# Kernel tuning notes

Measured on AMD Instinct MI355X. Metric: run time of the kernel, lower is better.

## Reference

```python
import jax, jax.numpy as jnp
import numpy as np

RADIUS = 8
EPS = 0.01


def _xdiff(h, r):
    # box-sum along H (axis 2) from cumsum via shifted-slice differences
    l = h[:, :, r:2 * r + 1]
    m = h[:, :, 2 * r + 1:] - h[:, :, :-2 * r - 1]
    rr = h[:, :, -1:] - h[:, :, -2 * r - 1:-r - 1]
    return jnp.concatenate([l, m, rr], axis=2)


def _ydiff(h, r):
    # box-sum along W (axis 3)
    l = h[:, :, :, r:2 * r + 1]
    m = h[:, :, :, 2 * r + 1:] - h[:, :, :, :-2 * r - 1]
    rr = h[:, :, :, -1:] - h[:, :, :, -2 * r - 1:-r - 1]
    return jnp.concatenate([l, m, rr], axis=3)


def mean_filter(x, r):
    return _ydiff(jnp.cumsum(_xdiff(jnp.cumsum(x, axis=2), r), axis=3), r)


def setup_inputs() -> dict:
    key = jax.random.key(0)
    k1, k2 = jax.random.split(key)
    shape = (8, 3, 1024, 1024)
    x = jax.random.uniform(k1, shape, dtype=jnp.float32)
    y = jax.random.uniform(k2, shape, dtype=jnp.float32)
    return {"x": x, "y": y}


def reference(x, y):
    r = RADIUS
    b, c, h, w = x.shape
    mask = jnp.ones((1, 1, h, w), dtype=x.dtype)
    nump = mean_filter(mask, r)  # per-pixel window counts (handles borders)
    x_mean = mean_filter(x, r) / nump
    y_mean = mean_filter(y, r) / nump
    xy_cov = mean_filter(x * y, r) / nump - x_mean * y_mean
    x_var = mean_filter(x * x, r) / nump - x_mean * x_mean
    a = xy_cov / (x_var + EPS)
    a_mean = mean_filter(a, r) / nump
    b_mean = mean_filter(y_mean - a * x_mean, r) / nump
    return a_mean * x + b_mean
```

## Files before the change

kernel.cpp:

```cpp
#include <hip/hip_runtime.h>


namespace {
constexpr int RAD  = 8;
constexpr int H    = 1024;
constexpr int W    = 1024;
constexpr int NSL  = 24;
constexpr int ROWS = 32;
constexpr int PW   = W + 2 * RAD;
constexpr float EPS_C = 0.01f;
constexpr int GRID = NSL * (H / ROWS);
constexpr size_t IMG = (size_t)NSL * H * W;
}

__device__ __forceinline__ float frcp(float v) { return __builtin_amdgcn_rcpf(v); }
__device__ __forceinline__ float4 z4() { return make_float4(0.f, 0.f, 0.f, 0.f); }

struct V4 { float4 x, y, xy, xx; };

__device__ __forceinline__ void vzero(V4& S) { S.x = z4(); S.y = z4(); S.xy = z4(); S.xx = z4(); }

__device__ __forceinline__ void vadd(V4& S, const float4 xv, const float4 yv) {
  S.x.x += xv.x; S.x.y += xv.y; S.x.z += xv.z; S.x.w += xv.w;
  S.y.x += yv.x; S.y.y += yv.y; S.y.z += yv.z; S.y.w += yv.w;
  S.xy.x += xv.x * yv.x; S.xy.y += xv.y * yv.y; S.xy.z += xv.z * yv.z; S.xy.w += xv.w * yv.w;
  S.xx.x += xv.x * xv.x; S.xx.y += xv.y * xv.y; S.xx.z += xv.z * xv.z; S.xx.w += xv.w * xv.w;
}

__device__ __forceinline__ void vsub(V4& S, const float4 xv, const float4 yv) {
  S.x.x -= xv.x; S.x.y -= xv.y; S.x.z -= xv.z; S.x.w -= xv.w;
  S.y.x -= yv.x; S.y.y -= yv.y; S.y.z -= yv.z; S.y.w -= yv.w;
  S.xy.x -= xv.x * yv.x; S.xy.y -= xv.y * yv.y; S.xy.z -= xv.z * yv.z; S.xy.w -= xv.w * yv.w;
  S.xx.x -= xv.x * xv.x; S.xx.y -= xv.y * xv.y; S.xx.z -= xv.z * xv.z; S.xx.w -= xv.w * xv.w;
}

__device__ __forceinline__ void map_block(int g, int& slice, int& r0) {
  const int xcd = g & 7;
  const int i = g >> 3;
  const int band = xcd * 4 + (i & 3);
  slice = i >> 2;
  r0 = band * ROWS;
}

__device__ __forceinline__ void hbox(const float* buf, int c0, float o[4]) {
  const float4 va = *reinterpret_cast<const float4*>(buf + c0);
  const float4 vb = *reinterpret_cast<const float4*>(buf + c0 + 4);
  const float4 vc = *reinterpret_cast<const float4*>(buf + c0 + 8);
  const float4 vd = *reinterpret_cast<const float4*>(buf + c0 + 12);
  const float4 ve = *reinterpret_cast<const float4*>(buf + c0 + 16);
  const float w[20] = {va.x, va.y, va.z, va.w, vb.x, vb.y, vb.z, vb.w,
                       vc.x, vc.y, vc.z, vc.w, vd.x, vd.y, vd.z, vd.w,
                       ve.x, ve.y, ve.z, ve.w};
  float s = w[0];
#pragma unroll
  for (int k = 1; k <= 16; ++k) s += w[k];
  o[0] = s;
  o[1] = o[0] - w[0] + w[17];
  o[2] = o[1] - w[1] + w[18];
  o[3] = o[2] - w[2] + w[19];
}

__device__ __forceinline__ float inv_cnt(int p) {
  int lo = p - RAD < 0 ? 0 : p - RAD;
  int hi = p + RAD > H - 1 ? H - 1 : p + RAD;
  return frcp((float)(hi - lo + 1));
}

__device__ __forceinline__ float4 ldrow(const float* __restrict__ s, int r, int c0) {
  return *reinterpret_cast<const float4*>(s + (size_t)r * W + c0);
}

__device__ __forceinline__ void publish(float* fbase, int c0, const V4& S) {
  *reinterpret_cast<float4*>(&fbase[0 * PW + RAD + c0]) = S.x;
  *reinterpret_cast<float4*>(&fbase[1 * PW + RAD + c0]) = S.y;
  *reinterpret_cast<float4*>(&fbase[2 * PW + RAD + c0]) = S.xy;
  *reinterpret_cast<float4*>(&fbase[3 * PW + RAD + c0]) = S.xx;
}

__device__ __forceinline__ void compute_ab(const float* fbase, int c0, float invcy,
                                           const float invcx[4], float av[4], float bv[4]) {
  float bx[4], by[4], bxy[4], bxx[4];
  hbox(fbase + 0 * PW, c0, bx);
  hbox(fbase + 1 * PW, c0, by);
  hbox(fbase + 2 * PW, c0, bxy);
  hbox(fbase + 3 * PW, c0, bxx);
#pragma unroll
  for (int j = 0; j < 4; ++j) {
    const float invN = invcy * invcx[j];
    const float mx = bx[j] * invN;
    const float my = by[j] * invN;
    const float cov = bxy[j] * invN - mx * my;
    const float var = bxx[j] * invN - mx * mx;
    const float a = cov * frcp(var + EPS_C);
    av[j] = a;
    bv[j] = my - a * mx;
  }
}

__device__ __forceinline__ void publish2(float* sbase, int c0, const float av[4], const float bv[4]) {
  *reinterpret_cast<float4*>(&sbase[RAD + c0]) = make_float4(av[0], av[1], av[2], av[3]);
  *reinterpret_cast<float4*>(&sbase[PW + RAD + c0]) = make_float4(bv[0], bv[1], bv[2], bv[3]);
}

__device__ __forceinline__ void hbox2(const float* sbase, int c0, float HA[4], float HB[4]) {
  hbox(sbase, c0, HA);
  hbox(sbase + PW, c0, HB);
}

__device__ __forceinline__ void setup_invcx(int c0, float invcx[4]) {
#pragma unroll
  for (int j = 0; j < 4; ++j) {
    const int c = c0 + j;
    const int cl = c - RAD < 0 ? 0 : c - RAD;
    const int ch = c + RAD > W - 1 ? W - 1 : c + RAD;
    invcx[j] = frcp((float)(ch - cl + 1));
  }
}

__global__ __launch_bounds__(256, 3) void k_ab(
    const float* __restrict__ x, const float* __restrict__ y,
    float* __restrict__ ag, float* __restrict__ bg) {
  __shared__ float stage[4 * PW];

  const int t = threadIdx.x;
  int slice, r0;
  map_block(blockIdx.x, slice, r0);
  const size_t soff = (size_t)slice * H * W;
  const float* xs = x + soff;
  const float* ys = y + soff;
  float* as = ag + soff;
  float* bs = bg + soff;
  const int c0 = t << 2;

  if (t < 64) {
    const int j = t >> 4, q = t & 15;
    const int pos = (q < 8) ? q : (W + RAD + (q - 8));
    stage[j * PW + pos] = 0.f;
  }

  float invcx[4];
  setup_invcx(c0, invcx);

  V4 SL; vzero(SL);
  {
    int lo = r0 - RAD < 0 ? 0 : r0 - RAD;
    for (int rr = lo; rr <= r0 + RAD; ++rr)
      vadd(SL, ldrow(xs, rr, c0), ldrow(ys, rr, c0));
  }
  __syncthreads();

  for (int p = r0; p < r0 + ROWS; ++p) {
    float4 xa = z4(), ya = z4(), xr = z4(), yr = z4();
    if (p + 9 <= H - 1) { xa = ldrow(xs, p + 9, c0); ya = ldrow(ys, p + 9, c0); }
    if (p - RAD >= 0)   { xr = ldrow(xs, p - RAD, c0); yr = ldrow(ys, p - RAD, c0); }

    publish(stage, c0, SL);
    __syncthreads();

    float av[4], bv[4];
    compute_ab(stage, c0, inv_cnt(p), invcx, av, bv);
    *reinterpret_cast<float4*>(as + (size_t)p * W + c0) = make_float4(av[0], av[1], av[2], av[3]);
    *reinterpret_cast<float4*>(bs + (size_t)p * W + c0) = make_float4(bv[0], bv[1], bv[2], bv[3]);

    vadd(SL, xa, ya);
    vsub(SL, xr, yr);
    __syncthreads();
  }
}

__global__ __launch_bounds__(256, 3) void k_out(
    const float* __restrict__ ag, const float* __restrict__ bg,
    const float* __restrict__ x, float* __restrict__ out) {
  __shared__ float srow[2 * PW];

  const int t = threadIdx.x;
  int slice, r0;
  map_block(blockIdx.x, slice, r0);
  const size_t soff = (size_t)slice * H * W;
  const float* as = ag + soff;
  const float* bs = bg + soff;
  const float* xs = x + soff;
  float* os = out + soff;
  const int c0 = t << 2;

  if (t < 32) {
    const int j = t >> 4, q = t & 15;
    const int pos = (q < 8) ? q : (W + RAD + (q - 8));
    srow[j * PW + pos] = 0.f;
  }

  float invcx[4];
  setup_invcx(c0, invcx);

  float4 Va = z4(), Vb = z4();
  {
    int lo = r0 - RAD < 0 ? 0 : r0 - RAD;
    for (int rr = lo; rr <= r0 + RAD; ++rr) {
      const float4 a4 = ldrow(as, rr, c0);
      const float4 b4 = ldrow(bs, rr, c0);
      Va.x += a4.x; Va.y += a4.y; Va.z += a4.z; Va.w += a4.w;
      Vb.x += b4.x; Vb.y += b4.y; Vb.z += b4.z; Vb.w += b4.w;
    }
  }
  __syncthreads();

  for (int k = r0; k < r0 + ROWS; ++k) {
    const float4 xk = ldrow(xs, k, c0);
    float4 aa = z4(), ba = z4(), ar = z4(), br = z4();
    if (k + 9 <= H - 1) { aa = ldrow(as, k + 9, c0); ba = ldrow(bs, k + 9, c0); }
    if (k - RAD >= 0)   { ar = ldrow(as, k - RAD, c0); br = ldrow(bs, k - RAD, c0); }

    *reinterpret_cast<float4*>(&srow[0 * PW + RAD + c0]) = Va;
    *reinterpret_cast<float4*>(&srow[1 * PW + RAD + c0]) = Vb;
    __syncthreads();

    float HA[4], HB[4];
    hbox(srow, c0, HA);
    hbox(srow + PW, c0, HB);

    const float invcy = inv_cnt(k);
    const float n0 = invcy * invcx[0], n1 = invcy * invcx[1];
    const float n2 = invcy * invcx[2], n3 = invcy * invcx[3];
    float4 o;
    o.x = HA[0] * n0 * xk.x + HB[0] * n0;
    o.y = HA[1] * n1 * xk.y + HB[1] * n1;
    o.z = HA[2] * n2 * xk.z + HB[2] * n2;
    o.w = HA[3] * n3 * xk.w + HB[3] * n3;
    *reinterpret_cast<float4*>(os + (size_t)k * W + c0) = o;

    Va.x += aa.x - ar.x; Va.y += aa.y - ar.y; Va.z += aa.z - ar.z; Va.w += aa.w - ar.w;
    Vb.x += ba.x - br.x; Vb.y += ba.y - br.y; Vb.z += ba.z - br.z; Vb.w += ba.w - br.w;
    __syncthreads();
  }
}

__global__ __launch_bounds__(256, 3) void k_fused(
    const float* __restrict__ x, const float* __restrict__ y, float* __restrict__ out) {
  __shared__ float stage[12 * PW];
  float* fL = stage;
  float* fG = stage + 4 * PW;
  float* sL = stage + 8 * PW;
  float* sG = stage + 10 * PW;

  const int t = threadIdx.x;
  int slice, r0;
  map_block(blockIdx.x, slice, r0);
  const size_t soff = (size_t)slice * H * W;
  const float* xs = x + soff;
  const float* ys = y + soff;
  float* os = out + soff;
  const int c0 = t << 2;

  if (t < 96) {
    const int j = t >> 3, tt = t & 7;
    stage[j * PW + tt] = 0.f;
    stage[j * PW + W + RAD + tt] = 0.f;
  }

  float invcx[4];
  setup_invcx(c0, invcx);

  const int cstart = (r0 - 9 < 0) ? 0 : (r0 - 9);
  V4 SL; vzero(SL);
  {
    int lo = cstart - RAD; if (lo < 0) lo = 0;
    for (int rr = lo; rr <= cstart + RAD; ++rr) {
      vadd(SL, ldrow(xs, rr, c0), ldrow(ys, rr, c0));
    }
  }
  V4 SG;
  if (r0 == 0) vzero(SG); else SG = SL;
  float4 Sa = z4(), Sb = z4();

  __syncthreads();

  for (int c = cstart; c <= r0 + 7; ++c) {
    const float4 xa = ldrow(xs, c + 9, c0), ya = ldrow(ys, c + 9, c0);
    float4 xr = z4(), yr = z4();
    if (c - RAD >= 0) { xr = ldrow(xs, c - RAD, c0); yr = ldrow(ys, c - RAD, c0); }

    publish(fL, c0, SL);
    __syncthreads();
    float av[4], bv[4];
    compute_ab(fL, c0, inv_cnt(c), invcx, av, bv);
    publish2(sL, c0, av, bv);
    __syncthreads();
    float HA[4], HB[4];
    hbox2(sL, c0, HA, HB);
    Sa.x += HA[0]; Sa.y += HA[1]; Sa.z += HA[2]; Sa.w += HA[3];
    Sb.x += HB[0]; Sb.y += HB[1]; Sb.z += HB[2]; Sb.w += HB[3];
    vadd(SL, xa, ya);
    vsub(SL, xr, yr);
    __syncthreads();
  }

  for (int k = r0; k < r0 + ROWS; ++k) {
    const float4 xk = ldrow(xs, k, c0), yk = ldrow(ys, k, c0);
    float4 xt = z4(), yt = z4(), xb = z4(), yb = z4();
    if (k + 17 < H)  { xt = ldrow(xs, k + 17, c0); yt = ldrow(ys, k + 17, c0); }
    if (k - 17 >= 0) { xb = ldrow(xs, k - 17, c0); yb = ldrow(ys, k - 17, c0); }

    publish(fL, c0, SL);
    publish(fG, c0, SG);
    __syncthreads();

    const int p = k + 8, q = k - 9;
    float avL[4], bvL[4], avG[4], bvG[4];
    compute_ab(fL, c0, inv_cnt(p), invcx, avL, bvL);
    compute_ab(fG, c0, inv_cnt(q), invcx, avG, bvG);
    publish2(sL, c0, avL, bvL);
    publish2(sG, c0, avG, bvG);
    __syncthreads();

    float HAL[4], HBL[4], HAG[4], HBG[4];
    hbox2(sL, c0, HAL, HBL);
    hbox2(sG, c0, HAG, HBG);
    if (p <= H - 1) {
      Sa.x += HAL[0]; Sa.y += HAL[1]; Sa.z += HAL[2]; Sa.w += HAL[3];
      Sb.x += HBL[0]; Sb.y += HBL[1]; Sb.z += HBL[2]; Sb.w += HBL[3];
    }
    if (q >= 0) {
      Sa.x -= HAG[0]; Sa.y -= HAG[1]; Sa.z -= HAG[2]; Sa.w -= HAG[3];
      Sb.x -= HBG[0]; Sb.y -= HBG[1]; Sb.z -= HBG[2]; Sb.w -= HBG[3];
    }

    const float invcy = inv_cnt(k);
    const float n0 = invcy * invcx[0], n1 = invcy * invcx[1];
    const float n2 = invcy * invcx[2], n3 = invcy * invcx[3];
    float4 o;
    o.x = Sa.x * n0 * xk.x + Sb.x * n0;
    o.y = Sa.y * n1 * xk.y + Sb.y * n1;
    o.z = Sa.z * n2 * xk.z + Sb.z * n2;
    o.w = Sa.w * n3 * xk.w + Sb.w * n3;
    *reinterpret_cast<float4*>(os + (size_t)k * W + c0) = o;

    vadd(SL, xt, yt);
    vsub(SL, xk, yk);
    vadd(SG, xk, yk);
    vsub(SG, xb, yb);
    __syncthreads();
  }
}

extern "C" void kernel_launch(void* const* d_in, const int* in_sizes, int n_in,
                              void* d_out, int out_size, void* d_ws, size_t ws_size,
                              hipStream_t stream) {
  const float* x = (const float*)d_in[0];
  const float* y = (const float*)d_in[1];
  float* out = (float*)d_out;
  const size_t need = 2 * IMG * sizeof(float);
  if (d_ws != nullptr && ws_size >= need) {
    float* ag = (float*)d_ws;
    float* bg = ag + IMG;
    k_ab<<<GRID, 256, 0, stream>>>(x, y, ag, bg);
    k_out<<<GRID, 256, 0, stream>>>(ag, bg, x, out);
  } else {
    k_fused<<<GRID, 256, 0, stream>>>(x, y, out);
  }
}
```

Before: 410.0 us.

## Use per-wave LDS staging with recomputed halos to drop block barriers

Rewrites k_ab and k_out so each 64-lane wave owns a private 256-column LDS strip plus 8-column halos on each side. Four lanes per wave keep their own vertical running sums for the halo columns, loading the extra global data they need. Because each wave only reads what it wrote, both per-row __syncthreads are removed. The cost is redundant halo loads and adds, and the code relies on lockstep execution within a wave for LDS visibility.

Result: no change. 406.9 us (-0.8%).

```diff
diff --git a/kernel.cpp b/kernel.cpp
--- a/kernel.cpp
+++ b/kernel.cpp
@@ -8,6 +8,7 @@
 constexpr int NSL  = 24;
 constexpr int ROWS = 32;
 constexpr int PW   = W + 2 * RAD;
+constexpr int WSTR = 272;
 constexpr float EPS_C = 0.01f;
 constexpr int GRID = NSL * (H / ROWS);
 constexpr size_t IMG = (size_t)NSL * H * W;
@@ -68,6 +69,200 @@
 
 __device__ __forceinline__ float4 ldrow(const float* __restrict__ s, int r, int c0) {
   return *reinterpret_cast<const float4*>(s + (size_t)r * W + c0);
+}
+
+__device__ __forceinline__ void compute_ab_w(const float* wb, int j0, float invcy,
+                                             const float invcx[4], float av[4], float bv[4]) {
+  float bx[4], by[4], bxy[4], bxx[4];
+  hbox(wb + 0 * WSTR, j0, bx);
+  hbox(wb + 1 * WSTR, j0, by);
+  hbox(wb + 2 * WSTR, j0, bxy);
+  hbox(wb + 3 * WSTR, j0, bxx);
+#pragma unroll
+  for (int j = 0; j < 4; ++j) {
+    const float invN = invcy * invcx[j];
+    const float mx = bx[j] * invN;
+    const float my = by[j] * invN;
+    const float cov = bxy[j] * invN - mx * my;
+    const float var = bxx[j] * invN - mx * mx;
+    const float a = cov * frcp(var + EPS_C);
+    av[j] = a;
+    bv[j] = my - a * mx;
+  }
+}
+
+__device__ __forceinline__ void setup_invcx(int c0, float invcx[4]) {
+#pragma unroll
+  for (int j = 0; j < 4; ++j) {
+    const int c = c0 + j;
+    const int cl = c - RAD < 0 ? 0 : c - RAD;
+    const int ch = c + RAD > W - 1 ? W - 1 : c + RAD;
+    invcx[j] = frcp((float)(ch - cl + 1));
+  }
+}
+
+__global__ __launch_bounds__(256, 3) void k_ab(
+    const float* __restrict__ x, const float* __restrict__ y,
+    float* __restrict__ ag, float* __restrict__ bg) {
+  __shared__ float stg[4][4][WSTR];
+
+  const int t = threadIdx.x;
+  const int lane = t & 63;
+  const int wid = t >> 6;
+  const int wavebase = wid << 8;
+  const int c0 = wavebase + (lane << 2);
+  const int j0 = lane << 2;
+
+  int slice, r0;
+  map_block(blockIdx.x, slice, r0);
+  const size_t soff = (size_t)slice * H * W;
+  const float* xs = x + soff;
+  const float* ys = y + soff;
+  float* as = ag + soff;
+  float* bs = bg + soff;
+
+  const int hc = (lane < 2) ? (wavebase - 8 + (lane << 2))
+                            : (wavebase + 256 + ((lane - 2) << 2));
+  const bool hvalid = (lane < 4) && hc >= 0 && hc < W;
+  const int hj = (lane < 2) ? (lane << 2) : (264 + ((lane - 2) << 2));
+
+  float invcx[4];
+  setup_invcx(c0, invcx);
+
+  V4 SL; vzero(SL);
+  V4 HS; vzero(HS);
+  {
+    int lo = r0 - RAD < 0 ? 0 : r0 - RAD;
+    for (int rr = lo; rr <= r0 + RAD; ++rr) {
+      vadd(SL, ldrow(xs, rr, c0), ldrow(ys, rr, c0));
+      if (hvalid) vadd(HS, ldrow(xs, rr, hc), ldrow(ys, rr, hc));
+    }
+  }
+
+  float* wb = &stg[wid][0][0];
+  for (int p = r0; p < r0 + ROWS; ++p) {
+    float4 xa = z4(), ya = z4(), xr = z4(), yr = z4();
+    float4 hxa = z4(), hya = z4(), hxr = z4(), hyr = z4();
+    if (p + 9 <= H - 1) {
+      xa = ldrow(xs, p + 9, c0); ya = ldrow(ys, p + 9, c0);
+      if (hvalid) { hxa = ldrow(xs, p + 9, hc); hya = ldrow(ys, p + 9, hc); }
+    }
+    if (p - RAD >= 0) {
+      xr = ldrow(xs, p - RAD, c0); yr = ldrow(ys, p - RAD, c0);
+      if (hvalid) { hxr = ldrow(xs, p - RAD, hc); hyr = ldrow(ys, p - RAD, hc); }
+    }
+
+    const int jp = 8 + (lane << 2);
+    *reinterpret_cast<float4*>(wb + 0 * WSTR + jp) = SL.x;
+    *reinterpret_cast<float4*>(wb + 1 * WSTR + jp) = SL.y;
+    *reinterpret_cast<float4*>(wb + 2 * WSTR + jp) = SL.xy;
+    *reinterpret_cast<float4*>(wb + 3 * WSTR + jp) = SL.xx;
+    if (lane < 4) {
+      *reinterpret_cast<float4*>(wb + 0 * WSTR + hj) = HS.x;
+      *reinterpret_cast<float4*>(wb + 1 * WSTR + hj) = HS.y;
+      *reinterpret_cast<float4*>(wb + 2 * WSTR + hj) = HS.xy;
+      *reinterpret_cast<float4*>(wb + 3 * WSTR + hj) = HS.xx;
+    }
+
+    float av[4], bv[4];
+    compute_ab_w(wb, j0, inv_cnt(p), invcx, av, bv);
+    *reinterpret_cast<float4*>(as + (size_t)p * W + c0) = make_float4(av[0], av[1], av[2], av[3]);
+    *reinterpret_cast<float4*>(bs + (size_t)p * W + c0) = make_float4(bv[0], bv[1], bv[2], bv[3]);
+
+    vadd(SL, xa, ya);
+    vsub(SL, xr, yr);
+    if (lane < 4) { vadd(HS, hxa, hya); vsub(HS, hxr, hyr); }
+  }
+}
+
+__global__ __launch_bounds__(256, 3) void k_out(
+    const float* __restrict__ ag, const float* __restrict__ bg,
+    const float* __restrict__ x, float* __restrict__ out) {
+  __shared__ float stg[4][2][WSTR];
+
+  const int t = threadIdx.x;
+  const int lane = t & 63;
+  const int wid = t >> 6;
+  const int wavebase = wid << 8;
+  const int c0 = wavebase + (lane << 2);
+  const int j0 = lane << 2;
+
+  int slice, r0;
+  map_block(blockIdx.x, slice, r0);
+  const size_t soff = (size_t)slice * H * W;
+  const float* as = ag + soff;
+  const float* bs = bg + soff;
+  const float* xs = x + soff;
+  float* os = out + soff;
+
+  const int hc = (lane < 2) ? (wavebase - 8 + (lane << 2))
+                            : (wavebase + 256 + ((lane - 2) << 2));
+  const bool hvalid = (lane < 4) && hc >= 0 && hc < W;
+  const int hj = (lane < 2) ? (lane << 2) : (264 + ((lane - 2) << 2));
+
+  float invcx[4];
+  setup_invcx(c0, invcx);
+
+  float4 Va = z4(), Vb = z4(), hVa = z4(), hVb = z4();
+  {
+    int lo = r0 - RAD < 0 ? 0 : r0 - RAD;
+    for (int rr = lo; rr <= r0 + RAD; ++rr) {
+      const float4 a4 = ldrow(as, rr, c0);
+      const float4 b4 = ldrow(bs, rr, c0);
+      Va.x += a4.x; Va.y += a4.y; Va.z += a4.z; Va.w += a4.w;
+      Vb.x += b4.x; Vb.y += b4.y; Vb.z += b4.z; Vb.w += b4.w;
+      if (hvalid) {
+        const float4 ha4 = ldrow(as, rr, hc);
+        const float4 hb4 = ldrow(bs, rr, hc);
+        hVa.x += ha4.x; hVa.y += ha4.y; hVa.z += ha4.z; hVa.w += ha4.w;
+        hVb.x += hb4.x; hVb.y += hb4.y; hVb.z += hb4.z; hVb.w += hb4.w;
+      }
+    }
+  }
+
+  float* wb = &stg[wid][0][0];
+  for (int k = r0; k < r0 + ROWS; ++k) {
+    const float4 xk = ldrow(xs, k, c0);
+    float4 aa = z4(), ba = z4(), ar = z4(), br = z4();
+    float4 haa = z4(), hba = z4(), har = z4(), hbr = z4();
+    if (k + 9 <= H - 1) {
+      aa = ldrow(as, k + 9, c0); ba = ldrow(bs, k + 9, c0);
+      if (hvalid) { haa = ldrow(as, k + 9, hc); hba = ldrow(bs, k + 9, hc); }
+    }
+    if (k - RAD >= 0) {
+      ar = ldrow(as, k - RAD, c0); br = ldrow(bs, k - RAD, c0);
+      if (hvalid) { har = ldrow(as, k - RAD, hc); hbr = ldrow(bs, k - RAD, hc); }
+    }
+
+    const int jp = 8 + (lane << 2);
+    *reinterpret_cast<float4*>(wb + 0 * WSTR + jp) = Va;
+    *reinterpret_cast<float4*>(wb + 1 * WSTR + jp) = Vb;
+    if (lane < 4) {
+      *reinterpret_cast<float4*>(wb + 0 * WSTR + hj) = hVa;
+      *reinterpret_cast<float4*>(wb + 1 * WSTR + hj) = hVb;
+    }
+
+    float HA[4], HB[4];
+    hbox(wb + 0 * WSTR, j0, HA);
+    hbox(wb + 1 * WSTR, j0, HB);
+
+    const float invcy = inv_cnt(k);
+    const float n0 = invcy * invcx[0], n1 = invcy * invcx[1];
+    const float n2 = invcy * invcx[2], n3 = invcy * invcx[3];
+    float4 o;
+    o.x = HA[0] * n0 * xk.x + HB[0] * n0;
+    o.y = HA[1] * n1 * xk.y + HB[1] * n1;
+    o.z = HA[2] * n2 * xk.z + HB[2] * n2;
+    o.w = HA[3] * n3 * xk.w + HB[3] * n3;
+    *reinterpret_cast<float4*>(os + (size_t)k * W + c0) = o;
+
+    Va.x += aa.x - ar.x; Va.y += aa.y - ar.y; Va.z += aa.z - ar.z; Va.w += aa.w - ar.w;
+    Vb.x += ba.x - br.x; Vb.y += ba.y - br.y; Vb.z += ba.z - br.z; Vb.w += ba.w - br.w;
+    if (hvalid) {
+      hVa.x += haa.x - har.x; hVa.y += haa.y - har.y; hVa.z += haa.z - har.z; hVa.w += haa.w - har.w;
+      hVb.x += hba.x - hbr.x; hVb.y += hba.y - hbr.y; hVb.z += hba.z - hbr.z; hVb.w += hba.w - hbr.w;
+    }
+  }
 }
 
 __device__ __forceinline__ void publish(float* fbase, int c0, const V4& S) {
@@ -107,133 +302,6 @@
   hbox(sbase + PW, c0, HB);
 }
 
-__device__ __forceinline__ void setup_invcx(int c0, float invcx[4]) {
-#pragma unroll
-  for (int j = 0; j < 4; ++j) {
-    const int c = c0 + j;
-    const int cl = c - RAD < 0 ? 0 : c - RAD;
-    const int ch = c + RAD > W - 1 ? W - 1 : c + RAD;
-    invcx[j] = frcp((float)(ch - cl + 1));
-  }
-}
-
-__global__ __launch_bounds__(256, 3) void k_ab(
-    const float* __restrict__ x, const float* __restrict__ y,
-    float* __restrict__ ag, float* __restrict__ bg) {
-  __shared__ float stage[4 * PW];
-
-  const int t = threadIdx.x;
-  int slice, r0;
-  map_block(blockIdx.x, slice, r0);
-  const size_t soff = (size_t)slice * H * W;
-  const float* xs = x + soff;
-  const float* ys = y + soff;
-  float* as = ag + soff;
-  float* bs = bg + soff;
-  const int c0 = t << 2;
-
-  if (t < 64) {
-    const int j = t >> 4, q = t & 15;
-    const int pos = (q < 8) ? q : (W + RAD + (q - 8));
-    stage[j * PW + pos] = 0.f;
-  }
-
-  float invcx[4];
-  setup_invcx(c0, invcx);
-
-  V4 SL; vzero(SL);
-  {
-    int lo = r0 - RAD < 0 ? 0 : r0 - RAD;
-    for (int rr = lo; rr <= r0 + RAD; ++rr)
-      vadd(SL, ldrow(xs, rr, c0), ldrow(ys, rr, c0));
-  }
-  __syncthreads();
-
-  for (int p = r0; p < r0 + ROWS; ++p) {
-    float4 xa = z4(), ya = z4(), xr = z4(), yr = z4();
-    if (p + 9 <= H - 1) { xa = ldrow(xs, p + 9, c0); ya = ldrow(ys, p + 9, c0); }
-    if (p - RAD >= 0)   { xr = ldrow(xs, p - RAD, c0); yr = ldrow(ys, p - RAD, c0); }
-
-    publish(stage, c0, SL);
-    __syncthreads();
-
-    float av[4], bv[4];
-    compute_ab(stage, c0, inv_cnt(p), invcx, av, bv);
-    *reinterpret_cast<float4*>(as + (size_t)p * W + c0) = make_float4(av[0], av[1], av[2], av[3]);
-    *reinterpret_cast<float4*>(bs + (size_t)p * W + c0) = make_float4(bv[0], bv[1], bv[2], bv[3]);
-
-    vadd(SL, xa, ya);
-    vsub(SL, xr, yr);
-    __syncthreads();
-  }
-}
-
-__global__ __launch_bounds__(256, 3) void k_out(
-    const float* __restrict__ ag, const float* __restrict__ bg,
-    const float* __restrict__ x, float* __restrict__ out) {
-  __shared__ float srow[2 * PW];
-
-  const int t = threadIdx.x;
-  int slice, r0;
-  map_block(blockIdx.x, slice, r0);
-  const size_t soff = (size_t)slice * H * W;
-  const float* as = ag + soff;
-  const float* bs = bg + soff;
-  const float* xs = x + soff;
-  float* os = out + soff;
-  const int c0 = t << 2;
-
-  if (t < 32) {
-    const int j = t >> 4, q = t & 15;
-    const int pos = (q < 8) ? q : (W + RAD + (q - 8));
-    srow[j * PW + pos] = 0.f;
-  }
-
-  float invcx[4];
-  setup_invcx(c0, invcx);
-
-  float4 Va = z4(), Vb = z4();
-  {
-    int lo = r0 - RAD < 0 ? 0 : r0 - RAD;
-    for (int rr = lo; rr <= r0 + RAD; ++rr) {
-      const float4 a4 = ldrow(as, rr, c0);
-      const float4 b4 = ldrow(bs, rr, c0);
-      Va.x += a4.x; Va.y += a4.y; Va.z += a4.z; Va.w += a4.w;
-      Vb.x += b4.x; Vb.y += b4.y; Vb.z += b4.z; Vb.w += b4.w;
-    }
-  }
-  __syncthreads();
-
-  for (int k = r0; k < r0 + ROWS; ++k) {
-    const float4 xk = ldrow(xs, k, c0);
-    float4 aa = z4(), ba = z4(), ar = z4(), br = z4();
-    if (k + 9 <= H - 1) { aa = ldrow(as, k + 9, c0); ba = ldrow(bs, k + 9, c0); }
-    if (k - RAD >= 0)   { ar = ldrow(as, k - RAD, c0); br = ldrow(bs, k - RAD, c0); }
-
-    *reinterpret_cast<float4*>(&srow[0 * PW + RAD + c0]) = Va;
-    *reinterpret_cast<float4*>(&srow[1 * PW + RAD + c0]) = Vb;
-    __syncthreads();
-
-    float HA[4], HB[4];
-    hbox(srow, c0, HA);
-    hbox(srow + PW, c0, HB);
-
-    const float invcy = inv_cnt(k);
-    const float n0 = invcy * invcx[0], n1 = invcy * invcx[1];
-    const float n2 = invcy * invcx[2], n3 = invcy * invcx[3];
-    float4 o;
-    o.x = HA[0] * n0 * xk.x + HB[0] * n0;
-    o.y = HA[1] * n1 * xk.y + HB[1] * n1;
-    o.z = HA[2] * n2 * xk.z + HB[2] * n2;
-    o.w = HA[3] * n3 * xk.w + HB[3] * n3;
-    *reinterpret_cast<float4*>(os + (size_t)k * W + c0) = o;
-
-    Va.x += aa.x - ar.x; Va.y += aa.y - ar.y; Va.z += aa.z - ar.z; Va.w += aa.w - ar.w;
-    Vb.x += ba.x - br.x; Vb.y += ba.y - br.y; Vb.z += ba.z - br.z; Vb.w += ba.w - br.w;
-    __syncthreads();
-  }
-}
-
 __global__ __launch_bounds__(256, 3) void k_fused(
     const float* __restrict__ x, const float* __restrict__ y, float* __restrict__ out) {
   __shared__ float stage[12 * PW];
```
